# Kernel tuning notes

Measured on AMD Instinct MI355X. Metric: run time of the kernel, lower is better.

The kernel has to match this reference:

```python
import jax, jax.numpy as jnp
import numpy as np

N_NODES = 100000
N_EDGES = 1600000
D_IN = 128
D_HID = 128
SCALE = 1.8
EPS = 1e-12


def setup_inputs() -> dict:
    key = jax.random.key(0)
    ks = jax.random.split(key, 7)
    x = jax.random.normal(ks[0], (N_NODES, D_IN), dtype=jnp.float32)
    W1 = jax.random.normal(ks[1], (D_HID, D_IN), dtype=jnp.float32) * 0.05
    b1 = jax.random.normal(ks[2], (D_HID,), dtype=jnp.float32) * 0.05
    W2 = jax.random.normal(ks[3], (D_HID, D_HID), dtype=jnp.float32) * 0.05
    b2 = jax.random.normal(ks[4], (D_HID,), dtype=jnp.float32) * 0.05
    src = jax.random.randint(ks[5], (N_EDGES,), 0, N_NODES, dtype=jnp.int64 if jax.config.jax_enable_x64 else jnp.int32)
    dst = jax.random.randint(ks[6], (N_EDGES,), 0, N_NODES, dtype=jnp.int64 if jax.config.jax_enable_x64 else jnp.int32)
    return {"x": x, "W1": W1, "b1": b1, "W2": W2, "b2": b2, "src": src, "dst": dst}


def reference(x, W1, b1, W2, b2, src, dst):
    N = x.shape[0]
    ones = jnp.ones((src.shape[0],), dtype=x.dtype)
    # GraphConv norm='both' degree normalizers (clamped to >=1 as in DGL)
    deg_out = jnp.maximum(jnp.zeros((N,), x.dtype).at[src].add(ones), 1.0)
    deg_in = jnp.maximum(jnp.zeros((N,), x.dtype).at[dst].add(ones), 1.0)
    norm_out = jax.lax.rsqrt(deg_out)[:, None]  # [N,1]
    norm_in = jax.lax.rsqrt(deg_in)[:, None]    # [N,1]

    def layer(h, W, b):
        # torch.nn.Linear: h @ W.T + b
        h = jnp.einsum('nd,kd->nk', h, W) + b
        # F.normalize(h, dim=1) * 1.8
        nrm = jnp.sqrt(jnp.sum(h * h, axis=1, keepdims=True))
        h = h / jnp.maximum(nrm, EPS) * SCALE
        # GraphConv (weight=False, bias=False, norm='both'):
        # D_out^{-1/2} -> sparse aggregate -> D_in^{-1/2}
        h = h * norm_out
        agg = jax.ops.segment_sum(h[src], dst, num_segments=N)
        return agg * norm_in

    h = layer(x, W1, b1)
    h = layer(h, W2, b2)
    return h
```

## Files before the change

kernel.cpp:

```cpp
#include <hip/hip_runtime.h>
#include <cstdint>
#include <cstddef>

#define D 128
#define NSCALE 1.8f
#define NEPS 1e-12f
#define EPB 2048
#define NBPAD 784
#define NLO 512
#define SCAP 9216
#define SRCB 23
#define SRCM 0x7FFFFF

typedef __attribute__((ext_vector_type(8))) short bf16x8;
typedef __attribute__((ext_vector_type(4))) float f32x4;

__device__ __forceinline__ ushort bf16_rtn(float f) {
    uint32_t u = __float_as_uint(f);
    u = u + 0x7FFFu + ((u >> 16) & 1u);
    return (ushort)(u >> 16);
}

__device__ __forceinline__ float blo(uint32_t u) { return __uint_as_float(u << 16); }
__device__ __forceinline__ float bhi(uint32_t u) { return __uint_as_float(u & 0xFFFF0000u); }

__global__ __launch_bounds__(256) void hist_high_kernel(const int* __restrict__ src,
                                                        const int* __restrict__ dst,
                                                        int* __restrict__ Hd,
                                                        int* __restrict__ Hs, int ne) {
    __shared__ int hd[256], hs[256];
    int t = threadIdx.x, b = blockIdx.x;
    hd[t] = 0; hs[t] = 0;
    __syncthreads();
    int base = b * EPB, end = min(ne, base + EPB);
    for (int i = base + t; i < end; i += 256) {
        atomicAdd(&hd[dst[i] >> 9], 1);
        atomicAdd(&hs[src[i] >> 9], 1);
    }
    __syncthreads();
    Hd[t * NBPAD + b] = hd[t];
    Hs[t * NBPAD + b] = hs[t];
}

__global__ __launch_bounds__(256) void scan_cols_kernel(int* __restrict__ Hd,
                                                        int* __restrict__ Hs,
                                                        int* __restrict__ total_d,
                                                        int* __restrict__ total_s, int nbk) {
    __shared__ int s[256];
    int* H = blockIdx.y ? Hs : Hd;
    int* tot = blockIdx.y ? total_s : total_d;
    int v = blockIdx.x, t = threadIdx.x;
    int base = v * NBPAD + 4 * t;
    int a0 = (4 * t + 0 < nbk) ? H[base + 0] : 0;
    int a1 = (4 * t + 1 < nbk) ? H[base + 1] : 0;
    int a2 = (4 * t + 2 < nbk) ? H[base + 2] : 0;
    int a3 = (4 * t + 3 < nbk) ? H[base + 3] : 0;
    int sum = a0 + a1 + a2 + a3;
    s[t] = sum;
    __syncthreads();
    #pragma unroll
    for (int off = 1; off < 256; off <<= 1) {
        int u = (t >= off) ? s[t - off] : 0;
        __syncthreads();
        s[t] += u;
        __syncthreads();
    }
    int excl = s[t] - sum;
    if (4 * t + 0 < nbk) H[base + 0] = excl;
    if (4 * t + 1 < nbk) H[base + 1] = excl + a0;
    if (4 * t + 2 < nbk) H[base + 2] = excl + a0 + a1;
    if (4 * t + 3 < nbk) H[base + 3] = excl + a0 + a1 + a2;
    if (t == 255) tot[v] = s[255];
}

__global__ __launch_bounds__(256) void scan_tot_kernel(const int* __restrict__ total_d,
                                                       const int* __restrict__ total_s,
                                                       int* __restrict__ Bd,
                                                       int* __restrict__ Bs, int hb) {
    __shared__ int s[256];
    const int* tot = blockIdx.x ? total_s : total_d;
    int* B = blockIdx.x ? Bs : Bd;
    int t = threadIdx.x;
    int val = (t < hb) ? tot[t] : 0;
    s[t] = val;
    __syncthreads();
    #pragma unroll
    for (int off = 1; off < 256; off <<= 1) {
        int u = (t >= off) ? s[t - off] : 0;
        __syncthreads();
        s[t] += u;
        __syncthreads();
    }
    if (t <= hb) B[t] = s[t] - val;
}

__global__ __launch_bounds__(256) void scatter_high_kernel(const int* __restrict__ src,
                                                           const int* __restrict__ dst,
                                                           const int* __restrict__ Hd,
                                                           const int* __restrict__ Hs,
                                                           const int* __restrict__ Bd,
                                                           const int* __restrict__ Bs,
                                                           uint32_t* __restrict__ spack,
                                                           ushort* __restrict__ ss_low,
                                                           int ne, int hb) {
    __shared__ int cur_d[256], cur_s[256];
    int t = threadIdx.x, b = blockIdx.x;
    if (t < hb) {
        cur_d[t] = Bd[t] + Hd[t * NBPAD + b];
        cur_s[t] = Bs[t] + Hs[t * NBPAD + b];
    }
    __syncthreads();
    int base = b * EPB, end = min(ne, base + EPB);
    for (int i = base + t; i < end; i += 256) {
        int d = dst[i], s = src[i];
        int pd = atomicAdd(&cur_d[d >> 9], 1);
        spack[pd] = ((uint32_t)(d & (NLO - 1)) << SRCB) | (uint32_t)s;
        int ps = atomicAdd(&cur_s[s >> 9], 1);
        ss_low[ps] = (ushort)(s & (NLO - 1));
    }
}

__global__ __launch_bounds__(1024) void bucket_sorthist_kernel(const uint32_t* __restrict__ spack,
                                                               const int* __restrict__ Bd,
                                                               const ushort* __restrict__ ss_low,
                                                               const int* __restrict__ Bs,
                                                               int* __restrict__ offs,
                                                               int* __restrict__ cnt_dst,
                                                               float* __restrict__ norm_in,
                                                               float* __restrict__ norm_out,
                                                               int* __restrict__ ssrc, int N) {
    __shared__ int h[NLO], sc[NLO], cur[NLO];
    __shared__ int stage[SCAP];
    int t = threadIdx.x, v = blockIdx.x;

    if (blockIdx.y == 1) {
        int beg = Bs[v], end = Bs[v + 1];
        if (t < NLO) h[t] = 0;
        __syncthreads();
        for (int i = beg + t; i < end; i += 1024) atomicAdd(&h[(int)ss_low[i]], 1);
        __syncthreads();
        int g = (v << 9) + t;
        if (t < NLO && g < N) norm_out[g] = rsqrtf((float)max(h[t], 1));
        return;
    }

    int beg = Bd[v], end = Bd[v + 1];
    int m = end - beg;
    if (t < NLO) h[t] = 0;
    __syncthreads();
    for (int i = beg + t; i < end; i += 1024) atomicAdd(&h[spack[i] >> SRCB], 1);
    __syncthreads();
    int cnt = 0;
    if (t < NLO) { cnt = h[t]; sc[t] = cnt; }
    __syncthreads();
    #pragma unroll
    for (int off = 1; off < NLO; off <<= 1) {
        int u = (t >= off && t < NLO) ? sc[t - off] : 0;
        __syncthreads();
        if (t < NLO) sc[t] += u;
        __syncthreads();
    }
    int excl = (t < NLO) ? (sc[t] - cnt) : 0;
    int g = (v << 9) + t;
    if (t < NLO && g < N) {
        offs[g] = beg + excl;
        cnt_dst[g] = cnt;
        norm_in[g] = rsqrtf((float)max(cnt, 1));
    }
    if (m <= SCAP) {
        if (t < NLO) cur[t] = excl;
        __syncthreads();
        for (int i = beg + t; i < end; i += 1024) {
            uint32_t p = spack[i];
            int pos = atomicAdd(&cur[p >> SRCB], 1);
            stage[pos] = (int)(p & SRCM);
        }
        __syncthreads();
        for (int j = t; j < m; j += 1024) ssrc[beg + j] = stage[j];
    } else {
        if (t < NLO) cur[t] = beg + excl;
        __syncthreads();
        for (int i = beg + t; i < end; i += 1024) {
            uint32_t p = spack[i];
            int pos = atomicAdd(&cur[p >> SRCB], 1);
            ssrc[pos] = (int)(p & SRCM);
        }
    }
}

__global__ __launch_bounds__(256) void mlp_fused_kernel(const float* __restrict__ X,
                                                        const float* __restrict__ W1,
                                                        const float* __restrict__ b1,
                                                        const float* __restrict__ W2,
                                                        const float* __restrict__ post,
                                                        ushort* __restrict__ Q,
                                                        ushort* __restrict__ Abuf, int N) {
    __shared__ ushort Wf[128 * 128];

    const int t = threadIdx.x;
    const int wave = t >> 6;
    const int lane = t & 63;
    const int q = lane >> 4;
    const int l16 = lane & 15;

    if (blockIdx.x == 0 && t < 32) {
        if (t < 16) ((uint4*)(Q    + (size_t)N * D))[t]      = make_uint4(0u, 0u, 0u, 0u);
        else        ((uint4*)(Abuf + (size_t)N * D))[t - 16] = make_uint4(0u, 0u, 0u, 0u);
    }

    #pragma unroll
    for (int it = 0; it < 8; ++it) {
        int f = t + 256 * it;
        int j = f >> 8;
        int p = (f >> 6) & 3;
        int ln = f & 63;
        int m = ln & 15;
        int row = 32 * (j >> 1) + 8 * (m >> 2) + 4 * (j & 1) + (m & 3);
        int k0 = 32 * p + 8 * (ln >> 4);
        const float* srcp = W1 + row * D + k0;
        float4 a0 = *(const float4*)(srcp);
        float4 a1 = *(const float4*)(srcp + 4);
        bf16x8 v;
        v[0] = (short)bf16_rtn(a0.x); v[1] = (short)bf16_rtn(a0.y);
        v[2] = (short)bf16_rtn(a0.z); v[3] = (short)bf16_rtn(a0.w);
        v[4] = (short)bf16_rtn(a1.x); v[5] = (short)bf16_rtn(a1.y);
        v[6] = (short)bf16_rtn(a1.z); v[7] = (short)bf16_rtn(a1.w);
        ((bf16x8*)Wf)[f] = v;
    }

    const int r0 = blockIdx.x * 128 + wave * 32;
    bf16x8 xhi[2][4], xlo[2][4];
    #pragma unroll
    for (int rt = 0; rt < 2; ++rt) {
        int row = r0 + rt * 16 + l16;
        bool ok = (row < N);
        const float* xr = X + (size_t)(ok ? row : 0) * D;
        #pragma unroll
        for (int p = 0; p < 4; ++p) {
            int k0 = 32 * p + 8 * q;
            float4 a0 = ok ? *(const float4*)(xr + k0)     : make_float4(0, 0, 0, 0);
            float4 a1 = ok ? *(const float4*)(xr + k0 + 4) : make_float4(0, 0, 0, 0);
            float fv[8] = {a0.x, a0.y, a0.z, a0.w, a1.x, a1.y, a1.z, a1.w};
            bf16x8 h, l;
            #pragma unroll
            for (int e = 0; e < 8; ++e) {
                uint32_t u = __float_as_uint(fv[e]);
                h[e] = (short)(u >> 16);
                float hf = __uint_as_float(u & 0xFFFF0000u);
                l[e] = (short)(__float_as_uint(fv[e] - hf) >> 16);
            }
            xhi[rt][p] = h;
            xlo[rt][p] = l;
        }
    }

    __syncthreads();

    f32x4 acc1[2][8];
    #pragma unroll
    for (int rt = 0; rt < 2; ++rt)
        #pragma unroll
        for (int j = 0; j < 8; ++j) acc1[rt][j] = (f32x4){0.f, 0.f, 0.f, 0.f};

    #pragma unroll
    for (int j = 0; j < 8; ++j) {
        #pragma unroll
        for (int p = 0; p < 4; ++p) {
            bf16x8 wf = ((bf16x8*)Wf)[(j * 4 + p) * 64 + lane];
            acc1[0][j] = __builtin_amdgcn_mfma_f32_16x16x32_bf16(wf, xhi[0][p], acc1[0][j], 0, 0, 0);
            acc1[0][j] = __builtin_amdgcn_mfma_f32_16x16x32_bf16(wf, xlo[0][p], acc1[0][j], 0, 0, 0);
            acc1[1][j] = __builtin_amdgcn_mfma_f32_16x16x32_bf16(wf, xhi[1][p], acc1[1][j], 0, 0, 0);
            acc1[1][j] = __builtin_amdgcn_mfma_f32_16x16x32_bf16(wf, xlo[1][p], acc1[1][j], 0, 0, 0);
        }
    }

    #pragma unroll
    for (int rt = 0; rt < 2; ++rt) {
        int node = r0 + rt * 16 + l16;
        float po = (node < N) ? post[node] : 0.f;
        float ss = 0.f;
        #pragma unroll
        for (int j = 0; j < 8; ++j) {
            const float4 bq = *(const float4*)(b1 + 32 * (j >> 1) + 8 * q + 4 * (j & 1));
            float v0 = acc1[rt][j][0] + bq.x; acc1[rt][j][0] = v0; ss += v0 * v0;
            float v1 = acc1[rt][j][1] + bq.y; acc1[rt][j][1] = v1; ss += v1 * v1;
            float v2 = acc1[rt][j][2] + bq.z; acc1[rt][j][2] = v2; ss += v2 * v2;
            float v3 = acc1[rt][j][3] + bq.w; acc1[rt][j][3] = v3; ss += v3 * v3;
        }
        ss += __shfl_xor(ss, 16);
        ss += __shfl_xor(ss, 32);
        float fsc = NSCALE / fmaxf(sqrtf(ss), NEPS) * po;
        #pragma unroll
        for (int j = 0; j < 8; ++j) {
            acc1[rt][j][0] *= fsc; acc1[rt][j][1] *= fsc;
            acc1[rt][j][2] *= fsc; acc1[rt][j][3] *= fsc;
        }
    }

    bf16x8 p2h[2][4], p2l[2][4];
    #pragma unroll
    for (int rt = 0; rt < 2; ++rt) {
        #pragma unroll
        for (int p = 0; p < 4; ++p) {
            bf16x8 hh, ll;
            #pragma unroll
            for (int e = 0; e < 8; ++e) {
                float vv = acc1[rt][2 * p + (e >> 2)][e & 3];
                uint32_t u = __float_as_uint(vv);
                hh[e] = (short)(u >> 16);
                float hf = __uint_as_float(u & 0xFFFF0000u);
                ll[e] = (short)(__float_as_uint(vv - hf) >> 16);
            }
            p2h[rt][p] = hh;
            p2l[rt][p] = ll;
        }
    }

    __syncthreads();
    #pragma unroll
    for (int it = 0; it < 8; ++it) {
        int f = t + 256 * it;
        int j = f >> 8;
        int p = (f >> 6) & 3;
        int ln = f & 63;
        int row = 16 * j + (ln & 15);
        int k0 = 32 * p + 8 * (ln >> 4);
        const float* srcp = W2 + row * D + k0;
        float4 a0 = *(const float4*)(srcp);
        float4 a1 = *(const float4*)(srcp + 4);
        bf16x8 v;
        v[0] = (short)bf16_rtn(a0.x); v[1] = (short)bf16_rtn(a0.y);
        v[2] = (short)bf16_rtn(a0.z); v[3] = (short)bf16_rtn(a0.w);
        v[4] = (short)bf16_rtn(a1.x); v[5] = (short)bf16_rtn(a1.y);
        v[6] = (short)bf16_rtn(a1.z); v[7] = (short)bf16_rtn(a1.w);
        ((bf16x8*)Wf)[f] = v;
    }
    __syncthreads();

    f32x4 acc2[2][8];
    #pragma unroll
    for (int rt = 0; rt < 2; ++rt)
        #pragma unroll
        for (int j = 0; j < 8; ++j) acc2[rt][j] = (f32x4){0.f, 0.f, 0.f, 0.f};

    #pragma unroll
    for (int j = 0; j < 8; ++j) {
        #pragma unroll
        for (int p = 0; p < 4; ++p) {
            bf16x8 wf = ((bf16x8*)Wf)[(j * 4 + p) * 64 + lane];
            acc2[0][j] = __builtin_amdgcn_mfma_f32_16x16x32_bf16(wf, p2h[0][p], acc2[0][j], 0, 0, 0);
            acc2[0][j] = __builtin_amdgcn_mfma_f32_16x16x32_bf16(wf, p2l[0][p], acc2[0][j], 0, 0, 0);
            acc2[1][j] = __builtin_amdgcn_mfma_f32_16x16x32_bf16(wf, p2h[1][p], acc2[1][j], 0, 0, 0);
            acc2[1][j] = __builtin_amdgcn_mfma_f32_16x16x32_bf16(wf, p2l[1][p], acc2[1][j], 0, 0, 0);
        }
    }

    #pragma unroll
    for (int rt = 0; rt < 2; ++rt) {
        int node = r0 + rt * 16 + l16;
        if (node < N) {
            ushort* qp = Q + (size_t)node * D + 4 * q;
            #pragma unroll
            for (int j = 0; j < 8; ++j) {
                ushort4 s4;
                s4.x = bf16_rtn(acc2[rt][j][0]);
                s4.y = bf16_rtn(acc2[rt][j][1]);
                s4.z = bf16_rtn(acc2[rt][j][2]);
                s4.w = bf16_rtn(acc2[rt][j][3]);
                *(ushort4*)(qp + 16 * j) = s4;
            }
        }
    }
}

__global__ __launch_bounds__(256) void agg_mid_kernel(const ushort* __restrict__ A,
                                                      const int* __restrict__ sorted_src,
                                                      const int* __restrict__ offs,
                                                      const int* __restrict__ cnt,
                                                      const float* __restrict__ norm_in,
                                                      const float* __restrict__ norm_out,
                                                      const float* __restrict__ b2,
                                                      ushort* __restrict__ Abuf, int N) {
    int wave = threadIdx.x >> 6;
    int n0 = (blockIdx.x * 4 + wave) * 2;
    if (n0 >= N) return;
    int lane = threadIdx.x & 63;
    int g = lane >> 4;
    int c = lane & 15;
    const ushort* Ac = A + c * 8;

    int n1 = n0 + 1;
    int beg0 = offs[n0], len0 = cnt[n0];
    int beg1 = 0, len1 = 0;
    if (n1 < N) { beg1 = offs[n1]; len1 = cnt[n1]; }
    int last0 = beg0 + len0 - 1;
    int last1 = beg1 + len1 - 1;

    float a0[8] = {0.f, 0.f, 0.f, 0.f, 0.f, 0.f, 0.f, 0.f};
    float a1[8] = {0.f, 0.f, 0.f, 0.f, 0.f, 0.f, 0.f, 0.f};

    int mx = max(len0, len1);
    for (int i = 0; i < mx; i += 16) {
        int idx[8];
        #pragma unroll
        for (int k = 0; k < 4; ++k) {
            int e = beg0 + i + g + 4 * k;
            int cl = max(min(e, last0), 0);
            idx[k] = sorted_src[cl];
            if (e > last0) idx[k] = N;
        }
        #pragma unroll
        for (int k = 0; k < 4; ++k) {
            int e = beg1 + i + g + 4 * k;
            int cl = max(min(e, last1), 0);
            idx[4 + k] = sorted_src[cl];
            if (e > last1) idx[4 + k] = N;
        }
        uint4 w[8];
        #pragma unroll
        for (int k = 0; k < 8; ++k) w[k] = *(const uint4*)(Ac + (size_t)idx[k] * D);
        #pragma unroll
        for (int k = 0; k < 4; ++k) {
            a0[0] += blo(w[k].x); a0[1] += bhi(w[k].x);
            a0[2] += blo(w[k].y); a0[3] += bhi(w[k].y);
            a0[4] += blo(w[k].z); a0[5] += bhi(w[k].z);
            a0[6] += blo(w[k].w); a0[7] += bhi(w[k].w);
        }
        #pragma unroll
        for (int k = 4; k < 8; ++k) {
            a1[0] += blo(w[k].x); a1[1] += bhi(w[k].x);
            a1[2] += blo(w[k].y); a1[3] += bhi(w[k].y);
            a1[4] += blo(w[k].z); a1[5] += bhi(w[k].z);
            a1[6] += blo(w[k].w); a1[7] += bhi(w[k].w);
        }
    }

    #pragma unroll
    for (int e = 0; e < 8; ++e) {
        a0[e] += __shfl_xor(a0[e], 16);
        a0[e] += __shfl_xor(a0[e], 32);
        a1[e] += __shfl_xor(a1[e], 16);
        a1[e] += __shfl_xor(a1[e], 32);
    }

    float4 bql = *(const float4*)(b2 + c * 8);
    float4 bqh = *(const float4*)(b2 + c * 8 + 4);
    float bb[8] = {bql.x, bql.y, bql.z, bql.w, bqh.x, bqh.y, bqh.z, bqh.w};

    {
        float ni = norm_in[n0];
        float y[8];
        float ss = 0.f;
        #pragma unroll
        for (int e = 0; e < 8; ++e) { y[e] = a0[e] * ni + bb[e]; ss += y[e] * y[e]; }
        ss += __shfl_xor(ss, 1); ss += __shfl_xor(ss, 2);
        ss += __shfl_xor(ss, 4); ss += __shfl_xor(ss, 8);
        float fsc = NSCALE / fmaxf(sqrtf(ss), NEPS) * norm_out[n0];
        if (g == 0) {
            ushort4 s0, s1;
            s0.x = bf16_rtn(y[0] * fsc); s0.y = bf16_rtn(y[1] * fsc);
            s0.z = bf16_rtn(y[2] * fsc); s0.w = bf16_rtn(y[3] * fsc);
            s1.x = bf16_rtn(y[4] * fsc); s1.y = bf16_rtn(y[5] * fsc);
            s1.z = bf16_rtn(y[6] * fsc); s1.w = bf16_rtn(y[7] * fsc);
            ushort* op = Abuf + (size_t)n0 * D + c * 8;
            *(ushort4*)(op) = s0;
            *(ushort4*)(op + 4) = s1;
        }
    }
    if (n1 < N) {
        float ni = norm_in[n1];
        float y[8];
        float ss = 0.f;
        #pragma unroll
        for (int e = 0; e < 8; ++e) { y[e] = a1[e] * ni + bb[e]; ss += y[e] * y[e]; }
        ss += __shfl_xor(ss, 1); ss += __shfl_xor(ss, 2);
        ss += __shfl_xor(ss, 4); ss += __shfl_xor(ss, 8);
        float fsc = NSCALE / fmaxf(sqrtf(ss), NEPS) * norm_out[n1];
        if (g == 0) {
            ushort4 s0, s1;
            s0.x = bf16_rtn(y[0] * fsc); s0.y = bf16_rtn(y[1] * fsc);
            s0.z = bf16_rtn(y[2] * fsc); s0.w = bf16_rtn(y[3] * fsc);
            s1.x = bf16_rtn(y[4] * fsc); s1.y = bf16_rtn(y[5] * fsc);
            s1.z = bf16_rtn(y[6] * fsc); s1.w = bf16_rtn(y[7] * fsc);
            ushort* op = Abuf + (size_t)n1 * D + c * 8;
            *(ushort4*)(op) = s0;
            *(ushort4*)(op + 4) = s1;
        }
    }
}

__global__ __launch_bounds__(256) void agg_kernel(const ushort* __restrict__ A,
                                                  const int* __restrict__ sorted_src,
                                                  const int* __restrict__ offs,
                                                  const int* __restrict__ cnt,
                                                  const float* __restrict__ norm_in,
                                                  float* __restrict__ out, int N) {
    int wave = threadIdx.x >> 6;
    int n0 = (blockIdx.x * 4 + wave) * 2;
    if (n0 >= N) return;
    int lane = threadIdx.x & 63;
    int g = lane >> 4;
    int c = lane & 15;
    const ushort* Ac = A + c * 8;

    int n1 = n0 + 1;
    int beg0 = offs[n0], len0 = cnt[n0];
    int beg1 = 0, len1 = 0;
    if (n1 < N) { beg1 = offs[n1]; len1 = cnt[n1]; }
    int last0 = beg0 + len0 - 1;
    int last1 = beg1 + len1 - 1;

    float a0[8] = {0.f, 0.f, 0.f, 0.f, 0.f, 0.f, 0.f, 0.f};
    float a1[8] = {0.f, 0.f, 0.f, 0.f, 0.f, 0.f, 0.f, 0.f};

    int mx = max(len0, len1);
    for (int i = 0; i < mx; i += 16) {
        int idx[8];
        #pragma unroll
        for (int k = 0; k < 4; ++k) {
            int e = beg0 + i + g + 4 * k;
            int cl = max(min(e, last0), 0);
            idx[k] = sorted_src[cl];
            if (e > last0) idx[k] = N;
        }
        #pragma unroll
        for (int k = 0; k < 4; ++k) {
            int e = beg1 + i + g + 4 * k;
            int cl = max(min(e, last1), 0);
            idx[4 + k] = sorted_src[cl];
            if (e > last1) idx[4 + k] = N;
        }
        uint4 w[8];
        #pragma unroll
        for (int k = 0; k < 8; ++k) w[k] = *(const uint4*)(Ac + (size_t)idx[k] * D);
        #pragma unroll
        for (int k = 0; k < 4; ++k) {
            a0[0] += blo(w[k].x); a0[1] += bhi(w[k].x);
            a0[2] += blo(w[k].y); a0[3] += bhi(w[k].y);
            a0[4] += blo(w[k].z); a0[5] += bhi(w[k].z);
            a0[6] += blo(w[k].w); a0[7] += bhi(w[k].w);
        }
        #pragma unroll
        for (int k = 4; k < 8; ++k) {
            a1[0] += blo(w[k].x); a1[1] += bhi(w[k].x);
            a1[2] += blo(w[k].y); a1[3] += bhi(w[k].y);
            a1[4] += blo(w[k].z); a1[5] += bhi(w[k].z);
            a1[6] += blo(w[k].w); a1[7] += bhi(w[k].w);
        }
    }

    #pragma unroll
    for (int e = 0; e < 8; ++e) {
        a0[e] += __shfl_xor(a0[e], 16);
        a0[e] += __shfl_xor(a0[e], 32);
        a1[e] += __shfl_xor(a1[e], 16);
        a1[e] += __shfl_xor(a1[e], 32);
    }

    if (g == 0) {
        float sc0 = norm_in[n0];
        float* op0 = out + (size_t)n0 * D + c * 8;
        *(float4*)(op0)     = make_float4(a0[0] * sc0, a0[1] * sc0, a0[2] * sc0, a0[3] * sc0);
        *(float4*)(op0 + 4) = make_float4(a0[4] * sc0, a0[5] * sc0, a0[6] * sc0, a0[7] * sc0);
        if (n1 < N) {
            float sc1 = norm_in[n1];
            float* op1 = out + (size_t)n1 * D + c * 8;
            *(float4*)(op1)     = make_float4(a1[0] * sc1, a1[1] * sc1, a1[2] * sc1, a1[3] * sc1);
            *(float4*)(op1 + 4) = make_float4(a1[4] * sc1, a1[5] * sc1, a1[6] * sc1, a1[7] * sc1);
        }
    }
}


extern "C" void kernel_launch(void* const* d_in, const int* in_sizes, int n_in,
                              void* d_out, int out_size, void* d_ws, size_t ws_size,
                              hipStream_t stream) {
    const float* x  = (const float*)d_in[0];
    const float* W1 = (const float*)d_in[1];
    const float* b1 = (const float*)d_in[2];
    const float* W2 = (const float*)d_in[3];
    const float* b2 = (const float*)d_in[4];
    const int* src  = (const int*)d_in[5];
    const int* dst  = (const int*)d_in[6];
    float* out = (float*)d_out;

    const int N  = in_sizes[0] / D;
    const int NE = in_sizes[5];
    const int NBK = (NE + EPB - 1) / EPB;
    const int HB  = (N + NLO - 1) / NLO;

    char* w = (char*)d_ws;
    auto take = [&](size_t bytes) { char* p = w; w += (bytes + 255) & ~(size_t)255; return p; };
    int*      Hd       = (int*)take((size_t)256 * NBPAD * 4);
    int*      Hs       = (int*)take((size_t)256 * NBPAD * 4);
    int*      total_d  = (int*)take(256 * 4);
    int*      total_s  = (int*)take(256 * 4);
    int*      Bd       = (int*)take((size_t)(HB + 1) * 4);
    int*      Bs       = (int*)take((size_t)(HB + 1) * 4);
    uint32_t* spack    = (uint32_t*)take((size_t)NE * 4);
    ushort*   ss_low   = (ushort*)take((size_t)NE * 2);
    int*      ssrc     = (int*)take((size_t)NE * 4);
    int*      offs     = (int*)take((size_t)N * 4);
    int*      cnt_dst  = (int*)take((size_t)N * 4);
    float*    norm_in  = (float*)take((size_t)N * 4);
    float*    norm_out = (float*)take((size_t)N * 4);
    ushort*   Qbuf     = (ushort*)take((size_t)(N + 1) * D * 2);
    ushort*   Abuf     = (ushort*)take((size_t)(N + 1) * D * 2);

    hist_high_kernel<<<NBK, 256, 0, stream>>>(src, dst, Hd, Hs, NE);
    scan_cols_kernel<<<dim3(HB, 2), 256, 0, stream>>>(Hd, Hs, total_d, total_s, NBK);
    scan_tot_kernel<<<2, 256, 0, stream>>>(total_d, total_s, Bd, Bs, HB);
    scatter_high_kernel<<<NBK, 256, 0, stream>>>(src, dst, Hd, Hs, Bd, Bs,
                                                 spack, ss_low, NE, HB);
    bucket_sorthist_kernel<<<dim3(HB, 2), 1024, 0, stream>>>(spack, Bd, ss_low, Bs,
                                                             offs, cnt_dst, norm_in,
                                                             norm_out, ssrc, N);

    const int mlp_blocks = (N + 127) / 128;
    const int agg_blocks = (N + 7) / 8;

    mlp_fused_kernel<<<mlp_blocks, 256, 0, stream>>>(x, W1, b1, W2, norm_out, Qbuf, Abuf, N);
    agg_mid_kernel<<<agg_blocks, 256, 0, stream>>>(Qbuf, ssrc, offs, cnt_dst,
                                                   norm_in, norm_out, b2, Abuf, N);
    agg_kernel<<<agg_blocks, 256, 0, stream>>>(Abuf, ssrc, offs, cnt_dst, norm_in, out, N);
}
```

Measured before the change: 323.5 us.

## Split scatter by key, stage bucket input in LDS, preload both MLP weights

```diff
diff --git a/kernel.cpp b/kernel.cpp
--- a/kernel.cpp
+++ b/kernel.cpp
@@ -103,20 +103,25 @@
                                                            uint32_t* __restrict__ spack,
                                                            ushort* __restrict__ ss_low,
                                                            int ne, int hb) {
-    __shared__ int cur_d[256], cur_s[256];
+    __shared__ int cur[256];
     int t = threadIdx.x, b = blockIdx.x;
-    if (t < hb) {
-        cur_d[t] = Bd[t] + Hd[t * NBPAD + b];
-        cur_s[t] = Bs[t] + Hs[t * NBPAD + b];
-    }
-    __syncthreads();
     int base = b * EPB, end = min(ne, base + EPB);
-    for (int i = base + t; i < end; i += 256) {
-        int d = dst[i], s = src[i];
-        int pd = atomicAdd(&cur_d[d >> 9], 1);
-        spack[pd] = ((uint32_t)(d & (NLO - 1)) << SRCB) | (uint32_t)s;
-        int ps = atomicAdd(&cur_s[s >> 9], 1);
-        ss_low[ps] = (ushort)(s & (NLO - 1));
+    if (blockIdx.y == 0) {
+        if (t < hb) cur[t] = Bd[t] + Hd[t * NBPAD + b];
+        __syncthreads();
+        for (int i = base + t; i < end; i += 256) {
+            int d = dst[i], s = src[i];
+            int pd = atomicAdd(&cur[d >> 9], 1);
+            spack[pd] = ((uint32_t)(d & (NLO - 1)) << SRCB) | (uint32_t)s;
+        }
+    } else {
+        if (t < hb) cur[t] = Bs[t] + Hs[t * NBPAD + b];
+        __syncthreads();
+        for (int i = base + t; i < end; i += 256) {
+            int s = src[i];
+            int ps = atomicAdd(&cur[s >> 9], 1);
+            ss_low[ps] = (ushort)(s & (NLO - 1));
+        }
     }
 }
 
@@ -130,6 +135,7 @@
                                                                float* __restrict__ norm_out,
                                                                int* __restrict__ ssrc, int N) {
     __shared__ int h[NLO], sc[NLO], cur[NLO];
+    __shared__ int inA[SCAP];
     __shared__ int stage[SCAP];
     int t = threadIdx.x, v = blockIdx.x;
 
@@ -146,9 +152,18 @@
 
     int beg = Bd[v], end = Bd[v + 1];
     int m = end - beg;
+    bool staged = (m <= SCAP);
+
     if (t < NLO) h[t] = 0;
-    __syncthreads();
-    for (int i = beg + t; i < end; i += 1024) atomicAdd(&h[spack[i] >> SRCB], 1);
+    if (staged) {
+        __syncthreads();
+        for (int i = beg + t; i < end; i += 1024) inA[i - beg] = (int)spack[i];
+        __syncthreads();
+        for (int i = t; i < m; i += 1024) atomicAdd(&h[((uint32_t)inA[i]) >> SRCB], 1);
+    } else {
+        __syncthreads();
+        for (int i = beg + t; i < end; i += 1024) atomicAdd(&h[spack[i] >> SRCB], 1);
+    }
     __syncthreads();
     int cnt = 0;
     if (t < NLO) { cnt = h[t]; sc[t] = cnt; }
@@ -167,11 +182,11 @@
         cnt_dst[g] = cnt;
         norm_in[g] = rsqrtf((float)max(cnt, 1));
     }
-    if (m <= SCAP) {
+    if (staged) {
         if (t < NLO) cur[t] = excl;
         __syncthreads();
-        for (int i = beg + t; i < end; i += 1024) {
-            uint32_t p = spack[i];
+        for (int i = t; i < m; i += 1024) {
+            uint32_t p = (uint32_t)inA[i];
             int pos = atomicAdd(&cur[p >> SRCB], 1);
             stage[pos] = (int)(p & SRCM);
         }
@@ -188,14 +203,15 @@
     }
 }
 
-__global__ __launch_bounds__(256) void mlp_fused_kernel(const float* __restrict__ X,
-                                                        const float* __restrict__ W1,
-                                                        const float* __restrict__ b1,
-                                                        const float* __restrict__ W2,
-                                                        const float* __restrict__ post,
-                                                        ushort* __restrict__ Q,
-                                                        ushort* __restrict__ Abuf, int N) {
-    __shared__ ushort Wf[128 * 128];
+__global__ __launch_bounds__(256, 2) void mlp_fused_kernel(const float* __restrict__ X,
+                                                           const float* __restrict__ W1,
+                                                           const float* __restrict__ b1,
+                                                           const float* __restrict__ W2,
+                                                           const float* __restrict__ post,
+                                                           ushort* __restrict__ Q,
+                                                           ushort* __restrict__ Abuf, int N) {
+    __shared__ ushort Wf1[128 * 128];
+    __shared__ ushort Wf2[128 * 128];
 
     const int t = threadIdx.x;
     const int wave = t >> 6;
@@ -215,17 +231,31 @@
         int p = (f >> 6) & 3;
         int ln = f & 63;
         int m = ln & 15;
-        int row = 32 * (j >> 1) + 8 * (m >> 2) + 4 * (j & 1) + (m & 3);
         int k0 = 32 * p + 8 * (ln >> 4);
-        const float* srcp = W1 + row * D + k0;
-        float4 a0 = *(const float4*)(srcp);
-        float4 a1 = *(const float4*)(srcp + 4);
-        bf16x8 v;
-        v[0] = (short)bf16_rtn(a0.x); v[1] = (short)bf16_rtn(a0.y);
-        v[2] = (short)bf16_rtn(a0.z); v[3] = (short)bf16_rtn(a0.w);
-        v[4] = (short)bf16_rtn(a1.x); v[5] = (short)bf16_rtn(a1.y);
-        v[6] = (short)bf16_rtn(a1.z); v[7] = (short)bf16_rtn(a1.w);
-        ((bf16x8*)Wf)[f] = v;
+        {
+            int row = 32 * (j >> 1) + 8 * (m >> 2) + 4 * (j & 1) + (m & 3);
+            const float* srcp = W1 + row * D + k0;
+            float4 a0 = *(const float4*)(srcp);
+            float4 a1 = *(const float4*)(srcp + 4);
+            bf16x8 v;
+            v[0] = (short)bf16_rtn(a0.x); v[1] = (short)bf16_rtn(a0.y);
+            v[2] = (short)bf16_rtn(a0.z); v[3] = (short)bf16_rtn(a0.w);
+            v[4] = (short)bf16_rtn(a1.x); v[5] = (short)bf16_rtn(a1.y);
+            v[6] = (short)bf16_rtn(a1.z); v[7] = (short)bf16_rtn(a1.w);
+            ((bf16x8*)Wf1)[f] = v;
+        }
+        {
+            int row = 16 * j + m;
+            const float* srcp = W2 + row * D + k0;
+            float4 a0 = *(const float4*)(srcp);
+            float4 a1 = *(const float4*)(srcp + 4);
+            bf16x8 v;
+            v[0] = (short)bf16_rtn(a0.x); v[1] = (short)bf16_rtn(a0.y);
+            v[2] = (short)bf16_rtn(a0.z); v[3] = (short)bf16_rtn(a0.w);
+            v[4] = (short)bf16_rtn(a1.x); v[5] = (short)bf16_rtn(a1.y);
+            v[6] = (short)bf16_rtn(a1.z); v[7] = (short)bf16_rtn(a1.w);
+            ((bf16x8*)Wf2)[f] = v;
+        }
     }
 
     const int r0 = blockIdx.x * 128 + wave * 32;
@@ -263,10 +293,10 @@
         for (int j = 0; j < 8; ++j) acc1[rt][j] = (f32x4){0.f, 0.f, 0.f, 0.f};
 
     #pragma unroll
-    for (int j = 0; j < 8; ++j) {
-        #pragma unroll
-        for (int p = 0; p < 4; ++p) {
-            bf16x8 wf = ((bf16x8*)Wf)[(j * 4 + p) * 64 + lane];
+    for (int p = 0; p < 4; ++p) {
+        #pragma unroll
+        for (int j = 0; j < 8; ++j) {
+            bf16x8 wf = ((bf16x8*)Wf1)[(j * 4 + p) * 64 + lane];
             acc1[0][j] = __builtin_amdgcn_mfma_f32_16x16x32_bf16(wf, xhi[0][p], acc1[0][j], 0, 0, 0);
             acc1[0][j] = __builtin_amdgcn_mfma_f32_16x16x32_bf16(wf, xlo[0][p], acc1[0][j], 0, 0, 0);
             acc1[1][j] = __builtin_amdgcn_mfma_f32_16x16x32_bf16(wf, xhi[1][p], acc1[1][j], 0, 0, 0);
@@ -297,46 +327,6 @@
         }
     }
 
-    bf16x8 p2h[2][4], p2l[2][4];
-    #pragma unroll
-    for (int rt = 0; rt < 2; ++rt) {
-        #pragma unroll
-        for (int p = 0; p < 4; ++p) {
-            bf16x8 hh, ll;
-            #pragma unroll
-            for (int e = 0; e < 8; ++e) {
-                float vv = acc1[rt][2 * p + (e >> 2)][e & 3];
-                uint32_t u = __float_as_uint(vv);
-                hh[e] = (short)(u >> 16);
-                float hf = __uint_as_float(u & 0xFFFF0000u);
-                ll[e] = (short)(__float_as_uint(vv - hf) >> 16);
-            }
-            p2h[rt][p] = hh;
-            p2l[rt][p] = ll;
-        }
-    }
-
-    __syncthreads();
-    #pragma unroll
-    for (int it = 0; it < 8; ++it) {
-        int f = t + 256 * it;
-        int j = f >> 8;
-        int p = (f >> 6) & 3;
-        int ln = f & 63;
-        int row = 16 * j + (ln & 15);
-        int k0 = 32 * p + 8 * (ln >> 4);
-        const float* srcp = W2 + row * D + k0;
-        float4 a0 = *(const float4*)(srcp);
-        float4 a1 = *(const float4*)(srcp + 4);
-        bf16x8 v;
-        v[0] = (short)bf16_rtn(a0.x); v[1] = (short)bf16_rtn(a0.y);
-        v[2] = (short)bf16_rtn(a0.z); v[3] = (short)bf16_rtn(a0.w);
-        v[4] = (short)bf16_rtn(a1.x); v[5] = (short)bf16_rtn(a1.y);
-        v[6] = (short)bf16_rtn(a1.z); v[7] = (short)bf16_rtn(a1.w);
-        ((bf16x8*)Wf)[f] = v;
-    }
-    __syncthreads();
-
     f32x4 acc2[2][8];
     #pragma unroll
     for (int rt = 0; rt < 2; ++rt)
@@ -344,14 +334,26 @@
         for (int j = 0; j < 8; ++j) acc2[rt][j] = (f32x4){0.f, 0.f, 0.f, 0.f};
 
     #pragma unroll
-    for (int j = 0; j < 8; ++j) {
-        #pragma unroll
-        for (int p = 0; p < 4; ++p) {
-            bf16x8 wf = ((bf16x8*)Wf)[(j * 4 + p) * 64 + lane];
-            acc2[0][j] = __builtin_amdgcn_mfma_f32_16x16x32_bf16(wf, p2h[0][p], acc2[0][j], 0, 0, 0);
-            acc2[0][j] = __builtin_amdgcn_mfma_f32_16x16x32_bf16(wf, p2l[0][p], acc2[0][j], 0, 0, 0);
-            acc2[1][j] = __builtin_amdgcn_mfma_f32_16x16x32_bf16(wf, p2h[1][p], acc2[1][j], 0, 0, 0);
-            acc2[1][j] = __builtin_amdgcn_mfma_f32_16x16x32_bf16(wf, p2l[1][p], acc2[1][j], 0, 0, 0);
+    for (int p = 0; p < 4; ++p) {
+        bf16x8 p2h0, p2l0, p2h1, p2l1;
+        #pragma unroll
+        for (int e = 0; e < 8; ++e) {
+            float v0 = acc1[0][2 * p + (e >> 2)][e & 3];
+            uint32_t u0 = __float_as_uint(v0);
+            p2h0[e] = (short)(u0 >> 16);
+            p2l0[e] = (short)(__float_as_uint(v0 - __uint_as_float(u0 & 0xFFFF0000u)) >> 16);
+            float v1 = acc1[1][2 * p + (e >> 2)][e & 3];
+            uint32_t u1 = __float_as_uint(v1);
+            p2h1[e] = (short)(u1 >> 16);
+            p2l1[e] = (short)(__float_as_uint(v1 - __uint_as_float(u1 & 0xFFFF0000u)) >> 16);
+        }
+        #pragma unroll
+        for (int j = 0; j < 8; ++j) {
+            bf16x8 wf = ((bf16x8*)Wf2)[(j * 4 + p) * 64 + lane];
+            acc2[0][j] = __builtin_amdgcn_mfma_f32_16x16x32_bf16(wf, p2h0, acc2[0][j], 0, 0, 0);
+            acc2[0][j] = __builtin_amdgcn_mfma_f32_16x16x32_bf16(wf, p2l0, acc2[0][j], 0, 0, 0);
+            acc2[1][j] = __builtin_amdgcn_mfma_f32_16x16x32_bf16(wf, p2h1, acc2[1][j], 0, 0, 0);
+            acc2[1][j] = __builtin_amdgcn_mfma_f32_16x16x32_bf16(wf, p2l1, acc2[1][j], 0, 0, 0);
         }
     }
 
@@ -610,8 +612,8 @@
     hist_high_kernel<<<NBK, 256, 0, stream>>>(src, dst, Hd, Hs, NE);
     scan_cols_kernel<<<dim3(HB, 2), 256, 0, stream>>>(Hd, Hs, total_d, total_s, NBK);
     scan_tot_kernel<<<2, 256, 0, stream>>>(total_d, total_s, Bd, Bs, HB);
-    scatter_high_kernel<<<NBK, 256, 0, stream>>>(src, dst, Hd, Hs, Bd, Bs,
-                                                 spack, ss_low, NE, HB);
+    scatter_high_kernel<<<dim3(NBK, 2), 256, 0, stream>>>(src, dst, Hd, Hs, Bd, Bs,
+                                                          spack, ss_low, NE, HB);
     bucket_sorthist_kernel<<<dim3(HB, 2), 1024, 0, stream>>>(spack, Bd, ss_low, Bs,
                                                              offs, cnt_dst, norm_in,
                                                              norm_out, ssrc, N);
```

Measured after the change: 306.6 us. -5.2%, faster.
